# Kernel optimization log

Measured on AMD Instinct MI355X. Metric: run time of the kernel, lower is better.

Reference implementation:

```python
import jax, jax.numpy as jnp
import numpy as np

WINDOW = 5  # window_size from init


def _avg_pool3d(x, k):
    # Matches F.avg_pool3d(kernel=k, stride=1, padding=k//2,
    # count_include_pad=True): windowed sum with zero padding / k^3.
    pad = k // 2
    s = jax.lax.reduce_window(
        x, 0.0, jax.lax.add,
        window_dimensions=(1, 1, k, k, k),
        window_strides=(1, 1, 1, 1, 1),
        padding=[(0, 0), (0, 0), (pad, pad), (pad, pad), (pad, pad)],
    )
    return s / float(k ** 3)


def setup_inputs() -> dict:
    key = jax.random.key(0)
    k1, k2 = jax.random.split(key)
    shape = (2, 1, 160, 192, 192)  # [B, C, D, H, W]
    source = jax.random.normal(k1, shape, dtype=jnp.float32)
    target = jax.random.normal(k2, shape, dtype=jnp.float32)
    return {"source": source, "target": target}


def reference(source, target):
    conv = lambda x: _avg_pool3d(x, WINDOW)
    src_mean = conv(source)
    tgt_mean = conv(target)
    src_var = conv(source * source) - src_mean * src_mean
    tgt_var = conv(target * target) - tgt_mean * tgt_mean
    cross = conv(source * target) - src_mean * tgt_mean
    lncc = cross * cross / (src_var * tgt_var + 1e-5)
    loss = 1.0 - jnp.mean(lncc)
    return jnp.nan_to_num(loss, nan=1.0, posinf=1.0, neginf=1.0)
```

## Files before the change

### kernel.cpp

```cpp
#include <hip/hip_runtime.h>
#include <math.h>

#define W_ 192
#define H_ 192
#define D_ 160
#define B_ 2
#define HW_ (H_ * W_)

#define TX 32
#define TY 16
#define HY 20
#define RAWP 41
#define RSP  33
#define CHUNK 20
#define PLANES (CHUNK + 4)
#define GX 6
#define GY 12
#define GZ 16
#define NBLK (GX * GY * GZ)
#define NTOT 11796480.0f

__global__ __launch_bounds__(256) void lncc_main(const float* __restrict__ src,
                                                 const float* __restrict__ tgt,
                                                 float* __restrict__ partial) {
    __shared__ float rawS[2][HY][RAWP];
    __shared__ float rawT[2][HY][RAWP];
    __shared__ float rsS [2][HY][RSP];
    __shared__ float rsT [2][HY][RSP];
    __shared__ float rsS2[2][HY][RSP];
    __shared__ float rsT2[2][HY][RSP];
    __shared__ float rsST[2][HY][RSP];
    __shared__ float wsum[4];

    const int tid = threadIdx.x;
    const int bz  = blockIdx.z;
    const int b   = bz >> 3;
    const int z0  = (bz & 7) * CHUNK;
    const int bx0 = blockIdx.x * TX - 4;
    const int by0 = blockIdx.y * TY - 2;

    const int  sr  = tid / 10;
    const int  sc4 = tid - sr * 10;
    const int  sc  = sc4 * 4;
    const int  sgx = bx0 + sc;
    const int  sgy = by0 + sr;
    const bool sW  = (tid < 200);
    const bool sOk = sW && ((unsigned)sgx < (unsigned)W_) && ((unsigned)sgy < (unsigned)H_);
    const size_t sOff = (size_t)sgy * W_ + (size_t)sgx;

    const int  p0y = tid >> 4;
    const int  p1y = p0y + 16;
    const int  xp  = tid & 15;
    const bool p1  = (tid < 64);
    const int  rc  = 2 * xp + 2;
    const int  wc  = 2 * xp;

    const int tx = tid & 31;
    const int y0 = (tid >> 5) * 2;

    float2 q0s=make_float2(0,0),q0t=make_float2(0,0),q0a=make_float2(0,0),q0b=make_float2(0,0),q0c=make_float2(0,0);
    float2 q1s=make_float2(0,0),q1t=make_float2(0,0),q1a=make_float2(0,0),q1b=make_float2(0,0),q1c=make_float2(0,0);
    float2 q2s=make_float2(0,0),q2t=make_float2(0,0),q2a=make_float2(0,0),q2b=make_float2(0,0),q2c=make_float2(0,0);
    float2 q3s=make_float2(0,0),q3t=make_float2(0,0),q3a=make_float2(0,0),q3b=make_float2(0,0),q3c=make_float2(0,0);
    float2 q4s=make_float2(0,0),q4t=make_float2(0,0),q4a=make_float2(0,0),q4b=make_float2(0,0),q4c=make_float2(0,0);
    float2 zS=make_float2(0,0),zT=make_float2(0,0),zA=make_float2(0,0),zB=make_float2(0,0),zC=make_float2(0,0);
    float lsum = 0.0f;

    auto phase2 = [&](int rbuf, int j) {
        float2 yS, yT, yA, yB, yC;
        {
            const float* p = &rsS[rbuf][y0][tx];
            float l0=p[0], l1=p[RSP], l2=p[2*RSP], l3=p[3*RSP], l4=p[4*RSP], l5=p[5*RSP];
            float m = l1 + l2 + l3 + l4;
            yS.x = l0 + m;  yS.y = m + l5;
        }
        {
            const float* p = &rsT[rbuf][y0][tx];
            float l0=p[0], l1=p[RSP], l2=p[2*RSP], l3=p[3*RSP], l4=p[4*RSP], l5=p[5*RSP];
            float m = l1 + l2 + l3 + l4;
            yT.x = l0 + m;  yT.y = m + l5;
        }
        {
            const float* p = &rsS2[rbuf][y0][tx];
            float l0=p[0], l1=p[RSP], l2=p[2*RSP], l3=p[3*RSP], l4=p[4*RSP], l5=p[5*RSP];
            float m = l1 + l2 + l3 + l4;
            yA.x = l0 + m;  yA.y = m + l5;
        }
        {
            const float* p = &rsT2[rbuf][y0][tx];
            float l0=p[0], l1=p[RSP], l2=p[2*RSP], l3=p[3*RSP], l4=p[4*RSP], l5=p[5*RSP];
            float m = l1 + l2 + l3 + l4;
            yB.x = l0 + m;  yB.y = m + l5;
        }
        {
            const float* p = &rsST[rbuf][y0][tx];
            float l0=p[0], l1=p[RSP], l2=p[2*RSP], l3=p[3*RSP], l4=p[4*RSP], l5=p[5*RSP];
            float m = l1 + l2 + l3 + l4;
            yC.x = l0 + m;  yC.y = m + l5;
        }
        zS.x += yS.x - q0s.x;  zS.y += yS.y - q0s.y;
        zT.x += yT.x - q0t.x;  zT.y += yT.y - q0t.y;
        zA.x += yA.x - q0a.x;  zA.y += yA.y - q0a.y;
        zB.x += yB.x - q0b.x;  zB.y += yB.y - q0b.y;
        zC.x += yC.x - q0c.x;  zC.y += yC.y - q0c.y;
        q0s=q1s; q0t=q1t; q0a=q1a; q0b=q1b; q0c=q1c;
        q1s=q2s; q1t=q2t; q1a=q2a; q1b=q2b; q1c=q2c;
        q2s=q3s; q2t=q3t; q2a=q3a; q2b=q3b; q2c=q3c;
        q3s=q4s; q3t=q4t; q3a=q4a; q3b=q4b; q3c=q4c;
        q4s=yS;  q4t=yT;  q4a=yA;  q4b=yB;  q4c=yC;
        if (j >= 4) {
            const float inv = 1.0f / 125.0f;
            {
                float ms = zS.x * inv, mt = zT.x * inv;
                float vs = fmaf(-ms, ms, zA.x * inv);
                float vt = fmaf(-mt, mt, zB.x * inv);
                float cr = fmaf(-ms, mt, zC.x * inv);
                float den = fmaf(vs, vt, 1e-5f);
                lsum = fmaf(cr * cr, __builtin_amdgcn_rcpf(den), lsum);
            }
            {
                float ms = zS.y * inv, mt = zT.y * inv;
                float vs = fmaf(-ms, ms, zA.y * inv);
                float vt = fmaf(-mt, mt, zB.y * inv);
                float cr = fmaf(-ms, mt, zC.y * inv);
                float den = fmaf(vs, vt, 1e-5f);
                lsum = fmaf(cr * cr, __builtin_amdgcn_rcpf(den), lsum);
            }
        }
    };

    auto rowsum = [&](int buf, int row) {
        const float* pS = &rawS[buf][row][rc];
        const float* pT = &rawT[buf][row][rc];
        float v0=pS[0],v1=pS[1],v2=pS[2],v3=pS[3],v4=pS[4],v5=pS[5];
        float u0=pT[0],u1=pT[1],u2=pT[2],u3=pT[3],u4=pT[4],u5=pT[5];
        float m  = v1 + v2 + v3 + v4;
        float n  = u1 + u2 + u3 + u4;
        float qS = fmaf(v1,v1, fmaf(v2,v2, fmaf(v3,v3, v4*v4)));
        float qT = fmaf(u1,u1, fmaf(u2,u2, fmaf(u3,u3, u4*u4)));
        float qX = fmaf(v1,u1, fmaf(v2,u2, fmaf(v3,u3, v4*u4)));
        rsS [buf][row][wc]   = v0 + m;
        rsS [buf][row][wc+1] = m + v5;
        rsT [buf][row][wc]   = u0 + n;
        rsT [buf][row][wc+1] = n + u5;
        rsS2[buf][row][wc]   = fmaf(v0,v0,qS);
        rsS2[buf][row][wc+1] = fmaf(v5,v5,qS);
        rsT2[buf][row][wc]   = fmaf(u0,u0,qT);
        rsT2[buf][row][wc+1] = fmaf(u5,u5,qT);
        rsST[buf][row][wc]   = fmaf(v0,u0,qX);
        rsST[buf][row][wc+1] = fmaf(v5,u5,qX);
    };

    {
        float4 vS = make_float4(0,0,0,0), vT = make_float4(0,0,0,0);
        const int zp = z0 - 2;
        if (zp >= 0 && sOk) {
            const size_t base = (size_t)(b * D_ + zp) * (size_t)HW_;
            vS = *(const float4*)(src + base + sOff);
            vT = *(const float4*)(tgt + base + sOff);
        }
        if (sW) {
            rawS[0][sr][sc]=vS.x; rawS[0][sr][sc+1]=vS.y; rawS[0][sr][sc+2]=vS.z; rawS[0][sr][sc+3]=vS.w;
            rawT[0][sr][sc]=vT.x; rawT[0][sr][sc+1]=vT.y; rawT[0][sr][sc+2]=vT.z; rawT[0][sr][sc+3]=vT.w;
        }
    }

    for (int i = 0; i < PLANES; ++i) {
        const int buf = i & 1;
        __syncthreads();
        float4 vS = make_float4(0,0,0,0), vT = make_float4(0,0,0,0);
        const bool haveNext = (i + 1 < PLANES);
        const int  zpn = z0 - 1 + i;
        if (haveNext && zpn >= 0 && zpn < D_ && sOk) {
            const size_t base = (size_t)(b * D_ + zpn) * (size_t)HW_;
            vS = *(const float4*)(src + base + sOff);
            vT = *(const float4*)(tgt + base + sOff);
        }
        if (i >= 1) phase2(buf ^ 1, i - 1);
        rowsum(buf, p0y);
        if (p1) rowsum(buf, p1y);
        if (haveNext && sW) {
            rawS[buf^1][sr][sc]=vS.x; rawS[buf^1][sr][sc+1]=vS.y; rawS[buf^1][sr][sc+2]=vS.z; rawS[buf^1][sr][sc+3]=vS.w;
            rawT[buf^1][sr][sc]=vT.x; rawT[buf^1][sr][sc+1]=vT.y; rawT[buf^1][sr][sc+2]=vT.z; rawT[buf^1][sr][sc+3]=vT.w;
        }
    }
    __syncthreads();
    phase2((PLANES - 1) & 1, PLANES - 1);

    #pragma unroll
    for (int off = 32; off > 0; off >>= 1)
        lsum += __shfl_down(lsum, off, 64);
    if ((tid & 63) == 0) wsum[tid >> 6] = lsum;
    __syncthreads();
    if (tid == 0) {
        const int bid = (blockIdx.z * GY + blockIdx.y) * GX + blockIdx.x;
        partial[bid] = wsum[0] + wsum[1] + wsum[2] + wsum[3];
    }
}

__global__ __launch_bounds__(256) void lncc_finalize(const float* __restrict__ partial,
                                                     float* __restrict__ out) {
    __shared__ float ws[4];
    const int t = threadIdx.x;
    float s = 0.0f;
    for (int i = t; i < NBLK; i += 256) s += partial[i];
    #pragma unroll
    for (int off = 32; off > 0; off >>= 1) s += __shfl_down(s, off, 64);
    if ((t & 63) == 0) ws[t >> 6] = s;
    __syncthreads();
    if (t == 0) {
        float tot = ws[0] + ws[1] + ws[2] + ws[3];
        float loss = 1.0f - tot * (1.0f / NTOT);
        if (isnan(loss) || isinf(loss)) loss = 1.0f;
        *out = loss;
    }
}

extern "C" void kernel_launch(void* const* d_in, const int* in_sizes, int n_in,
                              void* d_out, int out_size, void* d_ws, size_t ws_size,
                              hipStream_t stream) {
    const float* src = (const float*)d_in[0];
    const float* tgt = (const float*)d_in[1];
    float* out = (float*)d_out;
    float* partial = (float*)d_ws;

    dim3 grid(GX, GY, GZ);
    dim3 block(256, 1, 1);
    lncc_main<<<grid, block, 0, stream>>>(src, tgt, partial);
    lncc_finalize<<<dim3(1), dim3(256), 0, stream>>>(partial, out);
}
```

Before: 159.3 us.

## Halve tile height to one output row per thread, doubling block count

Shrinks the per-block tile from 16 to 8 output rows (halo rows 20 to 12) and doubles the grid in Y. Each thread now computes one output row instead of two, dropping the float2 register queues and the second rowsum pass. This lowers registers and shared memory per block so more blocks can be resident. The cost is a larger share of halo work: loaded and row-summed halo rows rise relative to useful output, and fewer threads do useful loads.

```diff
diff --git a/kernel.cpp b/kernel.cpp
--- a/kernel.cpp
+++ b/kernel.cpp
@@ -8,14 +8,14 @@
 #define HW_ (H_ * W_)
 
 #define TX 32
-#define TY 16
-#define HY 20
+#define TY 8
+#define HY 12
 #define RAWP 41
 #define RSP  33
 #define CHUNK 20
 #define PLANES (CHUNK + 4)
 #define GX 6
-#define GY 12
+#define GY 24
 #define GZ 16
 #define NBLK (GX * GY * GZ)
 #define NTOT 11796480.0f
@@ -44,65 +44,51 @@
     const int  sc  = sc4 * 4;
     const int  sgx = bx0 + sc;
     const int  sgy = by0 + sr;
-    const bool sW  = (tid < 200);
+    const bool sW  = (tid < 120);
     const bool sOk = sW && ((unsigned)sgx < (unsigned)W_) && ((unsigned)sgy < (unsigned)H_);
     const size_t sOff = (size_t)sgy * W_ + (size_t)sgx;
 
     const int  p0y = tid >> 4;
-    const int  p1y = p0y + 16;
     const int  xp  = tid & 15;
-    const bool p1  = (tid < 64);
+    const bool pAct = (tid < 192);
     const int  rc  = 2 * xp + 2;
     const int  wc  = 2 * xp;
 
     const int tx = tid & 31;
-    const int y0 = (tid >> 5) * 2;
-
-    float2 q0s=make_float2(0,0),q0t=make_float2(0,0),q0a=make_float2(0,0),q0b=make_float2(0,0),q0c=make_float2(0,0);
-    float2 q1s=make_float2(0,0),q1t=make_float2(0,0),q1a=make_float2(0,0),q1b=make_float2(0,0),q1c=make_float2(0,0);
-    float2 q2s=make_float2(0,0),q2t=make_float2(0,0),q2a=make_float2(0,0),q2b=make_float2(0,0),q2c=make_float2(0,0);
-    float2 q3s=make_float2(0,0),q3t=make_float2(0,0),q3a=make_float2(0,0),q3b=make_float2(0,0),q3c=make_float2(0,0);
-    float2 q4s=make_float2(0,0),q4t=make_float2(0,0),q4a=make_float2(0,0),q4b=make_float2(0,0),q4c=make_float2(0,0);
-    float2 zS=make_float2(0,0),zT=make_float2(0,0),zA=make_float2(0,0),zB=make_float2(0,0),zC=make_float2(0,0);
+    const int y0 = tid >> 5;
+
+    float q0s=0,q0t=0,q0a=0,q0b=0,q0c=0;
+    float q1s=0,q1t=0,q1a=0,q1b=0,q1c=0;
+    float q2s=0,q2t=0,q2a=0,q2b=0,q2c=0;
+    float q3s=0,q3t=0,q3a=0,q3b=0,q3c=0;
+    float q4s=0,q4t=0,q4a=0,q4b=0,q4c=0;
+    float zS=0,zT=0,zA=0,zB=0,zC=0;
     float lsum = 0.0f;
 
     auto phase2 = [&](int rbuf, int j) {
-        float2 yS, yT, yA, yB, yC;
+        float yS,yT,yA,yB,yC;
         {
             const float* p = &rsS[rbuf][y0][tx];
-            float l0=p[0], l1=p[RSP], l2=p[2*RSP], l3=p[3*RSP], l4=p[4*RSP], l5=p[5*RSP];
-            float m = l1 + l2 + l3 + l4;
-            yS.x = l0 + m;  yS.y = m + l5;
+            yS = p[0] + p[RSP] + p[2*RSP] + p[3*RSP] + p[4*RSP];
         }
         {
             const float* p = &rsT[rbuf][y0][tx];
-            float l0=p[0], l1=p[RSP], l2=p[2*RSP], l3=p[3*RSP], l4=p[4*RSP], l5=p[5*RSP];
-            float m = l1 + l2 + l3 + l4;
-            yT.x = l0 + m;  yT.y = m + l5;
+            yT = p[0] + p[RSP] + p[2*RSP] + p[3*RSP] + p[4*RSP];
         }
         {
             const float* p = &rsS2[rbuf][y0][tx];
-            float l0=p[0], l1=p[RSP], l2=p[2*RSP], l3=p[3*RSP], l4=p[4*RSP], l5=p[5*RSP];
-            float m = l1 + l2 + l3 + l4;
-            yA.x = l0 + m;  yA.y = m + l5;
+            yA = p[0] + p[RSP] + p[2*RSP] + p[3*RSP] + p[4*RSP];
         }
         {
             const float* p = &rsT2[rbuf][y0][tx];
-            float l0=p[0], l1=p[RSP], l2=p[2*RSP], l3=p[3*RSP], l4=p[4*RSP], l5=p[5*RSP];
-            float m = l1 + l2 + l3 + l4;
-            yB.x = l0 + m;  yB.y = m + l5;
+            yB = p[0] + p[RSP] + p[2*RSP] + p[3*RSP] + p[4*RSP];
         }
         {
             const float* p = &rsST[rbuf][y0][tx];
-            float l0=p[0], l1=p[RSP], l2=p[2*RSP], l3=p[3*RSP], l4=p[4*RSP], l5=p[5*RSP];
-            float m = l1 + l2 + l3 + l4;
-            yC.x = l0 + m;  yC.y = m + l5;
-        }
-        zS.x += yS.x - q0s.x;  zS.y += yS.y - q0s.y;
-        zT.x += yT.x - q0t.x;  zT.y += yT.y - q0t.y;
-        zA.x += yA.x - q0a.x;  zA.y += yA.y - q0a.y;
-        zB.x += yB.x - q0b.x;  zB.y += yB.y - q0b.y;
-        zC.x += yC.x - q0c.x;  zC.y += yC.y - q0c.y;
+            yC = p[0] + p[RSP] + p[2*RSP] + p[3*RSP] + p[4*RSP];
+        }
+        zS += yS - q0s;  zT += yT - q0t;  zA += yA - q0a;
+        zB += yB - q0b;  zC += yC - q0c;
         q0s=q1s; q0t=q1t; q0a=q1a; q0b=q1b; q0c=q1c;
         q1s=q2s; q1t=q2t; q1a=q2a; q1b=q2b; q1c=q2c;
         q2s=q3s; q2t=q3t; q2a=q3a; q2b=q3b; q2c=q3c;
@@ -110,22 +96,12 @@
         q4s=yS;  q4t=yT;  q4a=yA;  q4b=yB;  q4c=yC;
         if (j >= 4) {
             const float inv = 1.0f / 125.0f;
-            {
-                float ms = zS.x * inv, mt = zT.x * inv;
-                float vs = fmaf(-ms, ms, zA.x * inv);
-                float vt = fmaf(-mt, mt, zB.x * inv);
-                float cr = fmaf(-ms, mt, zC.x * inv);
-                float den = fmaf(vs, vt, 1e-5f);
-                lsum = fmaf(cr * cr, __builtin_amdgcn_rcpf(den), lsum);
-            }
-            {
-                float ms = zS.y * inv, mt = zT.y * inv;
-                float vs = fmaf(-ms, ms, zA.y * inv);
-                float vt = fmaf(-mt, mt, zB.y * inv);
-                float cr = fmaf(-ms, mt, zC.y * inv);
-                float den = fmaf(vs, vt, 1e-5f);
-                lsum = fmaf(cr * cr, __builtin_amdgcn_rcpf(den), lsum);
-            }
+            float ms = zS * inv, mt = zT * inv;
+            float vs = fmaf(-ms, ms, zA * inv);
+            float vt = fmaf(-mt, mt, zB * inv);
+            float cr = fmaf(-ms, mt, zC * inv);
+            float den = fmaf(vs, vt, 1e-5f);
+            lsum = fmaf(cr * cr, __builtin_amdgcn_rcpf(den), lsum);
         }
     };
 
@@ -177,8 +153,7 @@
             vT = *(const float4*)(tgt + base + sOff);
         }
         if (i >= 1) phase2(buf ^ 1, i - 1);
-        rowsum(buf, p0y);
-        if (p1) rowsum(buf, p1y);
+        if (pAct && p0y < HY) rowsum(buf, p0y);
         if (haveNext && sW) {
             rawS[buf^1][sr][sc]=vS.x; rawS[buf^1][sr][sc+1]=vS.y; rawS[buf^1][sr][sc+2]=vS.z; rawS[buf^1][sr][sc+3]=vS.w;
             rawT[buf^1][sr][sc]=vT.x; rawT[buf^1][sr][sc+1]=vT.y; rawT[buf^1][sr][sc+2]=vT.z; rawT[buf^1][sr][sc+3]=vT.w;
```

Result: faster. 153.1 us (-3.9%).

## Shrink tiles to single-wavefront blocks and single-buffer row-sum staging

Applied to the files above, without the earlier changes.

Reduces each block to one 64-thread wavefront covering a 16x8 output tile, which quadruples the grid. Row-sum shared buffers become single-buffered, with an extra barrier per plane between the row-sum and column-sum phases. The cross-wave shared reduction is removed. The aim is more blocks for occupancy and latency hiding plus less shared memory per block. In exchange the halo overhead per output rises sharply: a 24x12 input tile feeds 16x8 outputs, so there are more redundant global loads and row-sum work, and the second barrier per plane serialises the two phases.

```diff
diff --git a/kernel.cpp b/kernel.cpp
--- a/kernel.cpp
+++ b/kernel.cpp
@@ -7,30 +7,30 @@
 #define B_ 2
 #define HW_ (H_ * W_)
 
-#define TX 32
-#define TY 16
-#define HY 20
-#define RAWP 41
-#define RSP  33
+#define TX 16
+#define TY 8
+#define HY 12
+#define SCOLS 24
+#define RAWP 25
+#define RSP  24
 #define CHUNK 20
 #define PLANES (CHUNK + 4)
-#define GX 6
-#define GY 12
+#define GX 12
+#define GY 24
 #define GZ 16
 #define NBLK (GX * GY * GZ)
 #define NTOT 11796480.0f
 
-__global__ __launch_bounds__(256) void lncc_main(const float* __restrict__ src,
-                                                 const float* __restrict__ tgt,
-                                                 float* __restrict__ partial) {
+__global__ __launch_bounds__(64) void lncc_main(const float* __restrict__ src,
+                                                const float* __restrict__ tgt,
+                                                float* __restrict__ partial) {
     __shared__ float rawS[2][HY][RAWP];
     __shared__ float rawT[2][HY][RAWP];
-    __shared__ float rsS [2][HY][RSP];
-    __shared__ float rsT [2][HY][RSP];
-    __shared__ float rsS2[2][HY][RSP];
-    __shared__ float rsT2[2][HY][RSP];
-    __shared__ float rsST[2][HY][RSP];
-    __shared__ float wsum[4];
+    __shared__ float rsS [HY][RSP];
+    __shared__ float rsT [HY][RSP];
+    __shared__ float rsS2[HY][RSP];
+    __shared__ float rsT2[HY][RSP];
+    __shared__ float rsST[HY][RSP];
 
     const int tid = threadIdx.x;
     const int bz  = blockIdx.z;
@@ -39,24 +39,26 @@
     const int bx0 = blockIdx.x * TX - 4;
     const int by0 = blockIdx.y * TY - 2;
 
-    const int  sr  = tid / 10;
-    const int  sc4 = tid - sr * 10;
-    const int  sc  = sc4 * 4;
-    const int  sgx = bx0 + sc;
-    const int  sgy = by0 + sr;
-    const bool sW  = (tid < 200);
-    const bool sOk = sW && ((unsigned)sgx < (unsigned)W_) && ((unsigned)sgy < (unsigned)H_);
-    const size_t sOff = (size_t)sgy * W_ + (size_t)sgx;
-
-    const int  p0y = tid >> 4;
-    const int  p1y = p0y + 16;
-    const int  xp  = tid & 15;
-    const bool p1  = (tid < 64);
-    const int  rc  = 2 * xp + 2;
-    const int  wc  = 2 * xp;
-
-    const int tx = tid & 31;
-    const int y0 = (tid >> 5) * 2;
+    const int  s0row = tid / 6,        s0c = (tid - s0row * 6) * 4;
+    const int  s1slt = 64 + tid;
+    const int  s1row = s1slt / 6,      s1c = (s1slt - s1row * 6) * 4;
+    const bool s1W   = (tid < 8);
+    const int  s0gx = bx0 + s0c,  s0gy = by0 + s0row;
+    const int  s1gx = bx0 + s1c,  s1gy = by0 + s1row;
+    const bool s0Ok = ((unsigned)s0gx < (unsigned)W_) && ((unsigned)s0gy < (unsigned)H_);
+    const bool s1Ok = s1W && ((unsigned)s1gx < (unsigned)W_) && ((unsigned)s1gy < (unsigned)H_);
+    const size_t s0Off = (size_t)s0gy * W_ + (size_t)s0gx;
+    const size_t s1Off = (size_t)s1gy * W_ + (size_t)s1gx;
+
+    const int  xp   = tid & 7;
+    const int  p0y  = tid >> 3;
+    const int  p1y  = 8 + (tid >> 3);
+    const bool p1   = (tid < 32);
+    const int  rc   = 2 * xp + 2;
+    const int  wc   = 2 * xp;
+
+    const int tx = tid & 15;
+    const int y0 = (tid >> 4) * 2;
 
     float2 q0s=make_float2(0,0),q0t=make_float2(0,0),q0a=make_float2(0,0),q0b=make_float2(0,0),q0c=make_float2(0,0);
     float2 q1s=make_float2(0,0),q1t=make_float2(0,0),q1a=make_float2(0,0),q1b=make_float2(0,0),q1c=make_float2(0,0);
@@ -66,34 +68,34 @@
     float2 zS=make_float2(0,0),zT=make_float2(0,0),zA=make_float2(0,0),zB=make_float2(0,0),zC=make_float2(0,0);
     float lsum = 0.0f;
 
-    auto phase2 = [&](int rbuf, int j) {
+    auto phase2 = [&](int j) {
         float2 yS, yT, yA, yB, yC;
         {
-            const float* p = &rsS[rbuf][y0][tx];
+            const float* p = &rsS[y0][tx];
             float l0=p[0], l1=p[RSP], l2=p[2*RSP], l3=p[3*RSP], l4=p[4*RSP], l5=p[5*RSP];
             float m = l1 + l2 + l3 + l4;
             yS.x = l0 + m;  yS.y = m + l5;
         }
         {
-            const float* p = &rsT[rbuf][y0][tx];
+            const float* p = &rsT[y0][tx];
             float l0=p[0], l1=p[RSP], l2=p[2*RSP], l3=p[3*RSP], l4=p[4*RSP], l5=p[5*RSP];
             float m = l1 + l2 + l3 + l4;
             yT.x = l0 + m;  yT.y = m + l5;
         }
         {
-            const float* p = &rsS2[rbuf][y0][tx];
+            const float* p = &rsS2[y0][tx];
             float l0=p[0], l1=p[RSP], l2=p[2*RSP], l3=p[3*RSP], l4=p[4*RSP], l5=p[5*RSP];
             float m = l1 + l2 + l3 + l4;
             yA.x = l0 + m;  yA.y = m + l5;
         }
         {
-            const float* p = &rsT2[rbuf][y0][tx];
+            const float* p = &rsT2[y0][tx];
             float l0=p[0], l1=p[RSP], l2=p[2*RSP], l3=p[3*RSP], l4=p[4*RSP], l5=p[5*RSP];
             float m = l1 + l2 + l3 + l4;
             yB.x = l0 + m;  yB.y = m + l5;
         }
         {
-            const float* p = &rsST[rbuf][y0][tx];
+            const float* p = &rsST[y0][tx];
             float l0=p[0], l1=p[RSP], l2=p[2*RSP], l3=p[3*RSP], l4=p[4*RSP], l5=p[5*RSP];
             float m = l1 + l2 + l3 + l4;
             yC.x = l0 + m;  yC.y = m + l5;
@@ -139,62 +141,73 @@
         float qS = fmaf(v1,v1, fmaf(v2,v2, fmaf(v3,v3, v4*v4)));
         float qT = fmaf(u1,u1, fmaf(u2,u2, fmaf(u3,u3, u4*u4)));
         float qX = fmaf(v1,u1, fmaf(v2,u2, fmaf(v3,u3, v4*u4)));
-        rsS [buf][row][wc]   = v0 + m;
-        rsS [buf][row][wc+1] = m + v5;
-        rsT [buf][row][wc]   = u0 + n;
-        rsT [buf][row][wc+1] = n + u5;
-        rsS2[buf][row][wc]   = fmaf(v0,v0,qS);
-        rsS2[buf][row][wc+1] = fmaf(v5,v5,qS);
-        rsT2[buf][row][wc]   = fmaf(u0,u0,qT);
-        rsT2[buf][row][wc+1] = fmaf(u5,u5,qT);
-        rsST[buf][row][wc]   = fmaf(v0,u0,qX);
-        rsST[buf][row][wc+1] = fmaf(v5,u5,qX);
+        rsS [row][wc]   = v0 + m;
+        rsS [row][wc+1] = m + v5;
+        rsT [row][wc]   = u0 + n;
+        rsT [row][wc+1] = n + u5;
+        rsS2[row][wc]   = fmaf(v0,v0,qS);
+        rsS2[row][wc+1] = fmaf(v5,v5,qS);
+        rsT2[row][wc]   = fmaf(u0,u0,qT);
+        rsT2[row][wc+1] = fmaf(u5,u5,qT);
+        rsST[row][wc]   = fmaf(v0,u0,qX);
+        rsST[row][wc+1] = fmaf(v5,u5,qX);
     };
 
+    auto stageWrite = [&](int buf, const float4& v0S, const float4& v0T,
+                          const float4& v1S, const float4& v1T) {
+        rawS[buf][s0row][s0c]=v0S.x; rawS[buf][s0row][s0c+1]=v0S.y;
+        rawS[buf][s0row][s0c+2]=v0S.z; rawS[buf][s0row][s0c+3]=v0S.w;
+        rawT[buf][s0row][s0c]=v0T.x; rawT[buf][s0row][s0c+1]=v0T.y;
+        rawT[buf][s0row][s0c+2]=v0T.z; rawT[buf][s0row][s0c+3]=v0T.w;
+        if (s1W) {
+            rawS[buf][s1row][s1c]=v1S.x; rawS[buf][s1row][s1c+1]=v1S.y;
+            rawS[buf][s1row][s1c+2]=v1S.z; rawS[buf][s1row][s1c+3]=v1S.w;
+            rawT[buf][s1row][s1c]=v1T.x; rawT[buf][s1row][s1c+1]=v1T.y;
+            rawT[buf][s1row][s1c+2]=v1T.z; rawT[buf][s1row][s1c+3]=v1T.w;
+        }
+    };
+
     {
-        float4 vS = make_float4(0,0,0,0), vT = make_float4(0,0,0,0);
+        float4 a0S=make_float4(0,0,0,0), a0T=make_float4(0,0,0,0);
+        float4 a1S=make_float4(0,0,0,0), a1T=make_float4(0,0,0,0);
         const int zp = z0 - 2;
-        if (zp >= 0 && sOk) {
+        if (zp >= 0) {
             const size_t base = (size_t)(b * D_ + zp) * (size_t)HW_;
-            vS = *(const float4*)(src + base + sOff);
-            vT = *(const float4*)(tgt + base + sOff);
-        }
-        if (sW) {
-            rawS[0][sr][sc]=vS.x; rawS[0][sr][sc+1]=vS.y; rawS[0][sr][sc+2]=vS.z; rawS[0][sr][sc+3]=vS.w;
-            rawT[0][sr][sc]=vT.x; rawT[0][sr][sc+1]=vT.y; rawT[0][sr][sc+2]=vT.z; rawT[0][sr][sc+3]=vT.w;
-        }
+            if (s0Ok) { a0S = *(const float4*)(src + base + s0Off);
+                        a0T = *(const float4*)(tgt + base + s0Off); }
+            if (s1Ok) { a1S = *(const float4*)(src + base + s1Off);
+                        a1T = *(const float4*)(tgt + base + s1Off); }
+        }
+        stageWrite(0, a0S, a0T, a1S, a1T);
     }
 
     for (int i = 0; i < PLANES; ++i) {
         const int buf = i & 1;
         __syncthreads();
-        float4 vS = make_float4(0,0,0,0), vT = make_float4(0,0,0,0);
+        float4 a0S=make_float4(0,0,0,0), a0T=make_float4(0,0,0,0);
+        float4 a1S=make_float4(0,0,0,0), a1T=make_float4(0,0,0,0);
         const bool haveNext = (i + 1 < PLANES);
         const int  zpn = z0 - 1 + i;
-        if (haveNext && zpn >= 0 && zpn < D_ && sOk) {
+        if (haveNext && zpn >= 0 && zpn < D_) {
             const size_t base = (size_t)(b * D_ + zpn) * (size_t)HW_;
-            vS = *(const float4*)(src + base + sOff);
-            vT = *(const float4*)(tgt + base + sOff);
-        }
-        if (i >= 1) phase2(buf ^ 1, i - 1);
+            if (s0Ok) { a0S = *(const float4*)(src + base + s0Off);
+                        a0T = *(const float4*)(tgt + base + s0Off); }
+            if (s1Ok) { a1S = *(const float4*)(src + base + s1Off);
+                        a1T = *(const float4*)(tgt + base + s1Off); }
+        }
         rowsum(buf, p0y);
         if (p1) rowsum(buf, p1y);
-        if (haveNext && sW) {
-            rawS[buf^1][sr][sc]=vS.x; rawS[buf^1][sr][sc+1]=vS.y; rawS[buf^1][sr][sc+2]=vS.z; rawS[buf^1][sr][sc+3]=vS.w;
-            rawT[buf^1][sr][sc]=vT.x; rawT[buf^1][sr][sc+1]=vT.y; rawT[buf^1][sr][sc+2]=vT.z; rawT[buf^1][sr][sc+3]=vT.w;
-        }
-    }
-    __syncthreads();
-    phase2((PLANES - 1) & 1, PLANES - 1);
+        __syncthreads();
+        phase2(i);
+        if (haveNext) stageWrite(buf ^ 1, a0S, a0T, a1S, a1T);
+    }
 
     #pragma unroll
     for (int off = 32; off > 0; off >>= 1)
         lsum += __shfl_down(lsum, off, 64);
-    if ((tid & 63) == 0) wsum[tid >> 6] = lsum;
-    __syncthreads();
     if (tid == 0) {
         const int bid = (blockIdx.z * GY + blockIdx.y) * GX + blockIdx.x;
-        partial[bid] = wsum[0] + wsum[1] + wsum[2] + wsum[3];
+        partial[bid] = lsum;
     }
 }
 
@@ -225,7 +238,7 @@
     float* partial = (float*)d_ws;
 
     dim3 grid(GX, GY, GZ);
-    dim3 block(256, 1, 1);
+    dim3 block(64, 1, 1);
     lncc_main<<<grid, block, 0, stream>>>(src, tgt, partial);
     lncc_finalize<<<dim3(1), dim3(256), 0, stream>>>(partial, out);
 }
```

Result: slower. 185.3 us (+16.3%).
